# Optimization experiments

Measured on AMD Instinct MI355X. Metric: run time of the kernel, lower is better.

Reference implementation:

```python
import jax, jax.numpy as jnp
import numpy as np

B = 65536
NUM_INPUTS = 128
H0, H1 = 512, 512
K = 200
MIN_W = 0.001
MIN_H = 0.001
MIN_D = 0.001
EDGE_CONST = float(np.log(np.exp(1.0 - 0.001) - 1.0))  # in-place edge derivative value
LN_EPS = 1e-5


def setup_inputs() -> dict:
    key = jax.random.key(0)
    ks = jax.random.split(key, 10)
    f32 = jnp.float32
    inputs = jax.random.normal(ks[0], (B, NUM_INPUTS), dtype=f32)
    W1 = jax.random.normal(ks[1], (H0, NUM_INPUTS), dtype=f32) / np.sqrt(NUM_INPUTS)
    b1 = jnp.zeros((H0,), f32)
    g1 = jnp.ones((H0,), f32)
    be1 = jnp.zeros((H0,), f32)
    W2 = jax.random.normal(ks[2], (H1, H0), dtype=f32) / np.sqrt(H0)
    b2 = jnp.zeros((H1,), f32)
    g2 = jnp.ones((H1,), f32)
    be2 = jnp.zeros((H1,), f32)
    WV = jax.random.normal(ks[3], (3 * K - 1, H1), dtype=f32) / np.sqrt(H1)
    bV = jnp.zeros((3 * K - 1,), f32)
    Wa = jax.random.normal(ks[4], (1, H1), dtype=f32) / np.sqrt(H1)
    ba = jnp.zeros((1,), f32)
    Wb = jax.random.normal(ks[5], (1, H1), dtype=f32) / np.sqrt(H1)
    bb = jnp.zeros((1,), f32)
    return {"inputs": inputs, "W1": W1, "b1": b1, "g1": g1, "be1": be1,
            "W2": W2, "b2": b2, "g2": g2, "be2": be2,
            "WV": WV, "bV": bV, "Wa": Wa, "ba": ba, "Wb": Wb, "bb": bb}


def _layernorm(x, g, b):
    m = jnp.mean(x, axis=-1, keepdims=True)
    v = jnp.mean(jnp.square(x - m), axis=-1, keepdims=True)
    return (x - m) * jax.lax.rsqrt(v + LN_EPS) * g + b


def _spline_forward(inputs, W1, b1, g1, be1, W2, b2, g2, be2, WV, bV, Wa, ba, Wb, bb):
    x = jax.nn.relu(_layernorm(inputs @ W1.T + b1, g1, be1))
    x = jax.nn.relu(_layernorm(x @ W2.T + b2, g2, be2))
    sp = x @ WV.T + bV                      # [B, 3K-1]
    scale_a = jnp.exp(x @ Wa.T + ba)        # [B, 1]
    scale_b = x @ Wb.T + bb                 # [B, 1]

    Wp = jax.nn.softmax(sp[:, :K], axis=1)
    Hp = jax.nn.softmax(sp[:, K:2 * K], axis=1)
    Dp = sp[:, 2 * K:]                      # [B, K-1]
    Wp = MIN_W + (1.0 - MIN_W * K) * Wp
    Hp = MIN_H + (1.0 - MIN_H * K) * Hp
    Dp = MIN_D + jax.nn.softplus(Dp)
    bsz = inputs.shape[0]
    edge = jnp.full((bsz, 1), EDGE_CONST, dtype=inputs.dtype)
    D = jnp.concatenate([edge, Dp, edge], axis=-1)          # [B, K+1]

    zero = jnp.zeros((bsz, 1), dtype=inputs.dtype)
    cw = jnp.concatenate([zero, jnp.cumsum(Wp, axis=-1)], axis=-1)
    cw = cw.at[:, -1].set(1.0)                              # [B, K+1]
    widths = cw[:, 1:] - cw[:, :-1]                         # [B, K]
    ch = jnp.concatenate([zero, jnp.cumsum(Hp, axis=-1)], axis=-1)
    ch = scale_a * ch + scale_b                             # [B, K+1]
    heights = ch[:, 1:] - ch[:, :-1]                        # [B, K]

    tau = ((jnp.arange(K, dtype=inputs.dtype) + 0.5) / K)   # [K]
    tau = jnp.broadcast_to(tau, (bsz, K))

    # sum(tau >= bins) - 1 == searchsorted(bins, tau, side='right') - 1
    bin_idx = jax.vmap(lambda b, t: jnp.searchsorted(b, t, side='right'))(cw, tau) - 1

    ta = lambda a: jnp.take_along_axis(a, bin_idx, axis=-1)
    in_cw = ta(cw)
    in_w = ta(widths)
    in_ch = ta(ch)
    in_h = ta(heights)
    in_delta = ta(heights / widths)
    d0 = ta(D)
    d1 = ta(D[:, 1:])

    theta = (tau - in_cw) / in_w
    t1mt = theta * (1.0 - theta)
    numer = in_h * (in_delta * jnp.square(theta) + d0 * t1mt)
    denom = in_delta + (d0 + d1 - 2.0 * in_delta) * t1mt
    return in_ch + numer / denom            # [B, K]


def reference(inputs, W1, b1, g1, be1, W2, b2, g2, be2, WV, bV, Wa, ba, Wb, bb):
    return _spline_forward(inputs, W1, b1, g1, be1, W2, b2, g2, be2, WV, bV, Wa, ba, Wb, bb)
```

## Files before the change

### kernel.cpp

```cpp
#include <hip/hip_runtime.h>
#include <stdint.h>

typedef __bf16 bf16;
typedef __bf16 bf16x8 __attribute__((ext_vector_type(8)));
typedef __bf16 bf16x4 __attribute__((ext_vector_type(4)));
typedef float  f32x4  __attribute__((ext_vector_type(4)));
typedef uint32_t u32;

#define BATCH    65536
#define NCAT     640
#define SPSTRIDE 604

__device__ __forceinline__ void async16(const void* g, void* l) {
    __builtin_amdgcn_global_load_lds(
        (const u32 __attribute__((address_space(1)))*)g,
        (u32 __attribute__((address_space(3)))*)l,
        16, 0, 0);
}

__global__ __launch_bounds__(256) void prep_kernel(
    const float* W1, const float* W2, const float* WV,
    const float* bV, const float* Wa, const float* ba,
    const float* Wb, const float* bb, const float* inputs,
    bf16* w1b, bf16* w2b, bf16* wcat, float* bcat, bf16* xin)
{
    int idx = blockIdx.x * 256 + threadIdx.x;
    const int n1 = 512 * 128, n2 = 512 * 512, n3 = NCAT * 512;
    const int n5 = BATCH * 128 / 8;
    if (idx < n5) {
        const float4* src = (const float4*)(inputs + idx * 8);
        float4 v0 = src[0], v1 = src[1];
        bf16x8 h;
        h[0]=(bf16)v0.x; h[1]=(bf16)v0.y; h[2]=(bf16)v0.z; h[3]=(bf16)v0.w;
        h[4]=(bf16)v1.x; h[5]=(bf16)v1.y; h[6]=(bf16)v1.z; h[7]=(bf16)v1.w;
        *(bf16x8*)&xin[idx * 8] = h;
        return;
    }
    idx -= n5;
    if (idx < n1) { w1b[idx] = (bf16)W1[idx]; return; }
    idx -= n1;
    if (idx < n2) { w2b[idx] = (bf16)W2[idx]; return; }
    idx -= n2;
    if (idx < n3) {
        int n = idx >> 9, k = idx & 511;
        float v = 0.f;
        if (n < 599)       v = WV[n * 512 + k];
        else if (n == 599) v = Wa[k];
        else if (n == 600) v = Wb[k];
        wcat[idx] = (bf16)v;
        return;
    }
    idx -= n3;
    if (idx < NCAT) {
        float v = 0.f;
        if (idx < 599)       v = bV[idx];
        else if (idx == 599) v = ba[0];
        else if (idx == 600) v = bb[0];
        bcat[idx] = v;
    }
}

template <int KDIM>
__global__ __launch_bounds__(512, 4) void gemm_ln(
    const bf16* __restrict__ A, const bf16* __restrict__ W,
    const float* __restrict__ bias, const float* __restrict__ gamma,
    const float* __restrict__ beta, bf16* out)
{
    __shared__ __align__(16) char smem[8192 + 65536];
    char* Abase = smem;
    char* Bbase = smem + 8192;

    const int t = threadIdx.x;
    const int lane = t & 63, wid = t >> 6;
    const int wm = wid >> 2, wn = wid & 3;
    const int l16 = lane & 15, g16 = lane >> 4;
    const long row0 = (long)blockIdx.x * 64;
    constexpr int NT = KDIM / 32;

    f32x4 acc[2][8];
#pragma unroll
    for (int a = 0; a < 2; ++a)
#pragma unroll
        for (int b = 0; b < 8; ++b) acc[a][b] = (f32x4){0.f, 0.f, 0.f, 0.f};

    auto stageA = [&](int kt, int bi) {
        if (wid < 4) {
            int row = wid * 16 + (lane >> 2);
            const bf16* src = A + (row0 + row) * (long)KDIM + kt * 32 + (lane & 3) * 8;
            async16(src, Abase + bi * 4096 + wid * 1024);
        }
    };
    auto stageB = [&](int kt, int bi) {
#pragma unroll
        for (int c = 0; c < 4; ++c) {
            int call = wid * 4 + c;
            int row = call * 16 + (lane >> 2);
            const bf16* src = W + (long)row * KDIM + kt * 32 + (lane & 3) * 8;
            async16(src, Bbase + bi * 32768 + call * 1024);
        }
    };

    stageA(0, 0); stageB(0, 0);
    __syncthreads();

    for (int kt = 0; kt < NT; ++kt) {
        const int bi = kt & 1;
        if (kt + 1 < NT) { stageA(kt + 1, bi ^ 1); stageB(kt + 1, bi ^ 1); }
        const bf16* Ab = (const bf16*)(Abase + bi * 4096);
        const bf16* Bb = (const bf16*)(Bbase + bi * 32768);
        bf16x8 af[2];
#pragma unroll
        for (int fm = 0; fm < 2; ++fm)
            af[fm] = *(const bf16x8*)(Ab + (wm * 32 + fm * 16 + l16) * 32 + g16 * 8);
#pragma unroll
        for (int fn = 0; fn < 8; ++fn) {
            bf16x8 bv = *(const bf16x8*)(Bb + (wn * 128 + fn * 16 + l16) * 32 + g16 * 8);
            acc[0][fn] = __builtin_amdgcn_mfma_f32_16x16x32_bf16(af[0], bv, acc[0][fn], 0, 0, 0);
            acc[1][fn] = __builtin_amdgcn_mfma_f32_16x16x32_bf16(af[1], bv, acc[1][fn], 0, 0, 0);
        }
        __syncthreads();
    }

    float* Psum = (float*)Abase;
    float* Psq  = (float*)(Abase + 1024);
#pragma unroll
    for (int fm = 0; fm < 2; ++fm)
#pragma unroll
        for (int fn = 0; fn < 8; ++fn) {
            float bv = bias[wn * 128 + fn * 16 + l16];
#pragma unroll
            for (int i = 0; i < 4; ++i) acc[fm][fn][i] += bv;
        }
#pragma unroll
    for (int fm = 0; fm < 2; ++fm)
#pragma unroll
        for (int i = 0; i < 4; ++i) {
            float s = 0.f, q = 0.f;
#pragma unroll
            for (int fn = 0; fn < 8; ++fn) { float v = acc[fm][fn][i]; s += v; q += v * v; }
#pragma unroll
            for (int m = 1; m < 16; m <<= 1) { s += __shfl_xor(s, m); q += __shfl_xor(q, m); }
            if (l16 == 0) {
                int lr = wm * 32 + fm * 16 + g16 * 4 + i;
                Psum[lr * 4 + wn] = s; Psq[lr * 4 + wn] = q;
            }
        }
    __syncthreads();
#pragma unroll
    for (int fm = 0; fm < 2; ++fm)
#pragma unroll
        for (int i = 0; i < 4; ++i) {
            int lr = wm * 32 + fm * 16 + g16 * 4 + i;
            float s = Psum[lr * 4 + 0] + Psum[lr * 4 + 1] + Psum[lr * 4 + 2] + Psum[lr * 4 + 3];
            float q = Psq[lr * 4 + 0] + Psq[lr * 4 + 1] + Psq[lr * 4 + 2] + Psq[lr * 4 + 3];
            float mean = s * (1.f / 512.f);
            float var  = q * (1.f / 512.f) - mean * mean;
            float rstd = rsqrtf(var + 1e-5f);
            long grow = row0 + lr;
#pragma unroll
            for (int fn = 0; fn < 8; ++fn) {
                int col = wn * 128 + fn * 16 + l16;
                float o = (acc[fm][fn][i] - mean) * rstd * gamma[col] + beta[col];
                out[grow * 512 + col] = (bf16)fmaxf(o, 0.f);
            }
        }
}

__global__ __launch_bounds__(512, 4) void gemm_cat(
    const bf16* __restrict__ A, const bf16* __restrict__ W,
    const float* __restrict__ bcat, bf16* __restrict__ sp, float* __restrict__ ab)
{
    __shared__ __align__(16) char smem[16384 + 40960];
    char* Abase = smem;
    char* Bbase = smem + 16384;

    const int t = threadIdx.x;
    const int lane = t & 63, wid = t >> 6;
    const int wm = wid >> 2, wn = wid & 3;
    const int l16 = lane & 15, g16 = lane >> 4;
    const int nh  = blockIdx.x & 1;
    const long row0 = (long)(blockIdx.x >> 1) * 128;

    f32x4 acc[4][5];
#pragma unroll
    for (int a = 0; a < 4; ++a)
#pragma unroll
        for (int b = 0; b < 5; ++b) acc[a][b] = (f32x4){0.f, 0.f, 0.f, 0.f};

    auto stageA = [&](int kt, int bi) {
        int row = wid * 16 + (lane >> 2);
        const bf16* src = A + (row0 + row) * 512 + kt * 32 + (lane & 3) * 8;
        async16(src, Abase + bi * 8192 + wid * 1024);
    };
    auto stageB = [&](int kt, int bi) {
#pragma unroll
        for (int c = 0; c < 3; ++c) {
            int call = c * 8 + wid;
            if (call < 20) {
                int row = nh * 320 + call * 16 + (lane >> 2);
                const bf16* src = W + (long)row * 512 + kt * 32 + (lane & 3) * 8;
                async16(src, Bbase + bi * 20480 + call * 1024);
            }
        }
    };

    stageA(0, 0); stageB(0, 0);
    __syncthreads();

    for (int kt = 0; kt < 16; ++kt) {
        const int bi = kt & 1;
        if (kt < 15) { stageA(kt + 1, bi ^ 1); stageB(kt + 1, bi ^ 1); }
        const bf16* Ab = (const bf16*)(Abase + bi * 8192);
        const bf16* Bb = (const bf16*)(Bbase + bi * 20480);
        bf16x8 af[4];
#pragma unroll
        for (int fm = 0; fm < 4; ++fm)
            af[fm] = *(const bf16x8*)(Ab + (wm * 64 + fm * 16 + l16) * 32 + g16 * 8);
#pragma unroll
        for (int fn = 0; fn < 5; ++fn) {
            bf16x8 bv = *(const bf16x8*)(Bb + (wn * 80 + fn * 16 + l16) * 32 + g16 * 8);
#pragma unroll
            for (int fm = 0; fm < 4; ++fm)
                acc[fm][fn] = __builtin_amdgcn_mfma_f32_16x16x32_bf16(af[fm], bv, acc[fm][fn], 0, 0, 0);
        }
        __syncthreads();
    }

#pragma unroll
    for (int fn = 0; fn < 5; ++fn) {
        int col = nh * 320 + wn * 80 + fn * 16 + l16;
        float bv = (col <= 600) ? bcat[col] : 0.f;
#pragma unroll
        for (int fm = 0; fm < 4; ++fm)
#pragma unroll
            for (int i = 0; i < 4; ++i) {
                long grow = row0 + wm * 64 + fm * 16 + g16 * 4 + i;
                float v = acc[fm][fn][i] + bv;
                if (col < 599)       sp[grow * SPSTRIDE + col] = (bf16)v;
                else if (col == 599) ab[grow * 2 + 0] = v;
                else if (col == 600) ab[grow * 2 + 1] = v;
            }
    }
}

__global__ __launch_bounds__(256) void spline_kernel(
    const bf16* __restrict__ sp, const float* __restrict__ ab, float* __restrict__ out)
{
    __shared__ float S[4][816];
    const int t = threadIdx.x;
    const int lane = t & 63, wid = t >> 6;
    const long row = (long)blockIdx.x * 4 + wid;
    const bf16* spr = sp + row * SPSTRIDE;
    const bool act = lane < 50;
    const float EC = 0.53974247f;
    float* cw = &S[wid][0];
    float* ch = &S[wid][204];
    float* dd = &S[wid][408];
    int*   bx = (int*)&S[wid][612];

    const float sa = __expf(ab[row * 2 + 0]);
    const float sb = ab[row * 2 + 1];

    auto rng = [](float x) -> int {
        int v = (int)ceilf(fmaf(200.f, x, -0.5f));
        return v < 0 ? 0 : (v > 200 ? 200 : v);
    };

    float p0, p1, p2, p3;
    {
        float x0, x1, x2v, x3;
        if (act) {
            bf16x4 v = *(const bf16x4*)&spr[4 * lane];
            x0 = (float)v[0]; x1 = (float)v[1]; x2v = (float)v[2]; x3 = (float)v[3];
        } else { x0 = x1 = x2v = x3 = -1e30f; }
        float m = fmaxf(fmaxf(x0, x1), fmaxf(x2v, x3));
#pragma unroll
        for (int d = 1; d < 64; d <<= 1) m = fmaxf(m, __shfl_xor(m, d));
        float e0 = act ? __expf(x0 - m) : 0.f;
        float e1 = act ? __expf(x1 - m) : 0.f;
        float e2 = act ? __expf(x2v - m) : 0.f;
        float e3 = act ? __expf(x3 - m) : 0.f;
        float s = e0 + e1 + e2 + e3;
#pragma unroll
        for (int d = 1; d < 64; d <<= 1) s += __shfl_xor(s, d);
        float inv = 0.8f / s;
        p0 = act ? fmaf(e0, inv, 0.001f) : 0.f;
        p1 = act ? fmaf(e1, inv, 0.001f) : 0.f;
        p2 = act ? fmaf(e2, inv, 0.001f) : 0.f;
        p3 = act ? fmaf(e3, inv, 0.001f) : 0.f;
    }
    float c0 = p0, c1 = c0 + p1, c2 = c1 + p2, c3 = c2 + p3;
    float run = c3, ts = run;
#pragma unroll
    for (int d = 1; d < 64; d <<= 1) { float u = __shfl_up(ts, d); if (lane >= d) ts += u; }
    float excl  = ts - run;
    float nexcl = __shfl_down(excl, 1);
    float cwl0 = excl, cwl1 = excl + c0, cwl2 = excl + c1, cwl3 = excl + c2;

    float hp0, hp1, hp2, hp3;
    {
        float x0, x1, x2v, x3;
        if (act) {
            bf16x4 v = *(const bf16x4*)&spr[200 + 4 * lane];
            x0 = (float)v[0]; x1 = (float)v[1]; x2v = (float)v[2]; x3 = (float)v[3];
        } else { x0 = x1 = x2v = x3 = -1e30f; }
        float m = fmaxf(fmaxf(x0, x1), fmaxf(x2v, x3));
#pragma unroll
        for (int d = 1; d < 64; d <<= 1) m = fmaxf(m, __shfl_xor(m, d));
        float e0 = act ? __expf(x0 - m) : 0.f;
        float e1 = act ? __expf(x1 - m) : 0.f;
        float e2 = act ? __expf(x2v - m) : 0.f;
        float e3 = act ? __expf(x3 - m) : 0.f;
        float s = e0 + e1 + e2 + e3;
#pragma unroll
        for (int d = 1; d < 64; d <<= 1) s += __shfl_xor(s, d);
        float inv = 0.8f / s;
        hp0 = act ? fmaf(e0, inv, 0.001f) : 0.f;
        hp1 = act ? fmaf(e1, inv, 0.001f) : 0.f;
        hp2 = act ? fmaf(e2, inv, 0.001f) : 0.f;
        hp3 = act ? fmaf(e3, inv, 0.001f) : 0.f;
    }
    float hc0 = hp0, hc1 = hc0 + hp1, hc2 = hc1 + hp2, hc3 = hc2 + hp3;
    float hrun = hc3, hts = hrun;
#pragma unroll
    for (int d = 1; d < 64; d <<= 1) { float u = __shfl_up(hts, d); if (lane >= d) hts += u; }
    float hexcl = hts - hrun;
    float ch0 = fmaf(sa, hexcl, sb);
    float ch1 = fmaf(sa, hexcl + hc0, sb);
    float ch2 = fmaf(sa, hexcl + hc1, sb);
    float ch3 = fmaf(sa, hexcl + hc2, sb);

    float dv0, dv1, dv2, dv3;
    {
        float x0 = 0.f, x1 = 0.f, x2v = 0.f, x3 = 0.f;
        if (act) {
            bf16x4 v = *(const bf16x4*)&spr[400 + 4 * lane];
            x0 = (float)v[0]; x1 = (float)v[1]; x2v = (float)v[2]; x3 = (float)v[3];
        }
        auto spls = [](float x) {
            return fmaxf(x, 0.f) + __logf(1.f + __expf(-fabsf(x))) + 0.001f;
        };
        dv0 = spls(x0); dv1 = spls(x1); dv2 = spls(x2v); dv3 = spls(x3);
    }
    if (lane == 49) dv3 = EC;
    float dprev = __shfl_up(dv3, 1);
    if (lane == 0) dprev = EC;

    if (act) {
        *(f32x4*)&cw[4 * lane] = (f32x4){cwl0, cwl1, cwl2, cwl3};
        *(f32x4*)&ch[4 * lane] = (f32x4){ch0, ch1, ch2, ch3};
        *(f32x4*)&dd[4 * lane] = (f32x4){dprev, dv0, dv1, dv2};
    }
    if (lane == 49) {
        cw[200] = 1.0f;
        ch[200] = fmaf(sa, hts, sb);
        dd[200] = EC;
    }

    if (act) {
        int b0 = rng(cwl0), b1 = rng(cwl1), b2 = rng(cwl2), b3 = rng(cwl3);
        int b4 = (lane == 49) ? 200 : rng(nexcl);
        for (int j = b0; j < b1; ++j) bx[j] = 4 * lane;
        for (int j = b1; j < b2; ++j) bx[j] = 4 * lane + 1;
        for (int j = b2; j < b3; ++j) bx[j] = 4 * lane + 2;
        for (int j = b3; j < b4; ++j) bx[j] = 4 * lane + 3;
    }
    asm volatile("s_waitcnt lgkmcnt(0)" ::: "memory");

    if (act) {
        float* orow = out + (size_t)row * 200;
#pragma unroll
        for (int k = 0; k < 4; ++k) {
            int j = lane + 50 * k;
            int b = bx[j];
            float wl = cw[b], wr = cw[b + 1];
            float hl = ch[b], hr = ch[b + 1];
            float d0 = dd[b], d1 = dd[b + 1];
            float tau = ((float)j + 0.5f) * (1.f / 200.f);
            float w = wr - wl, h = hr - hl;
            float invw = 1.f / w;
            float delta = h * invw;
            float th = (tau - wl) * invw;
            float t1 = th * (1.f - th);
            float numer = h * fmaf(delta * th, th, d0 * t1);
            float denom = fmaf(d0 + d1 - 2.f * delta, t1, delta);
            orow[j] = hl + numer / denom;
        }
    }
}

extern "C" void kernel_launch(void* const* d_in, const int* in_sizes, int n_in,
                              void* d_out, int out_size, void* d_ws, size_t ws_size,
                              hipStream_t stream)
{
    const float* inputs = (const float*)d_in[0];
    const float* W1  = (const float*)d_in[1];
    const float* b1  = (const float*)d_in[2];
    const float* g1  = (const float*)d_in[3];
    const float* be1 = (const float*)d_in[4];
    const float* W2  = (const float*)d_in[5];
    const float* b2  = (const float*)d_in[6];
    const float* g2  = (const float*)d_in[7];
    const float* be2 = (const float*)d_in[8];
    const float* WV  = (const float*)d_in[9];
    const float* bV  = (const float*)d_in[10];
    const float* Wa  = (const float*)d_in[11];
    const float* ba  = (const float*)d_in[12];
    const float* Wb  = (const float*)d_in[13];
    const float* bb  = (const float*)d_in[14];
    float* out = (float*)d_out;

    char* ws = (char*)d_ws;
    bf16*  w1b  = (bf16*) (ws + 0);
    bf16*  w2b  = (bf16*) (ws + 131072);
    bf16*  wcat = (bf16*) (ws + 655360);
    float* bcat = (float*)(ws + 1310720);
    float* ab   = (float*)(ws + 1313280);
    bf16*  x    = (bf16*) (ws + 2097152);
    bf16*  spb  = (bf16*) (ws + 69206016);
    bf16*  xin  = (bf16*) (ws + 69206016);

    const int preptot = BATCH * 128 / 8 + 512 * 128 + 512 * 512 + NCAT * 512 + NCAT;
    prep_kernel<<<(preptot + 255) / 256, 256, 0, stream>>>(
        W1, W2, WV, bV, Wa, ba, Wb, bb, inputs, w1b, w2b, wcat, bcat, xin);

    gemm_ln<128><<<BATCH / 64, 512, 0, stream>>>(xin, w1b, b1, g1, be1, x);
    gemm_ln<512><<<BATCH / 64, 512, 0, stream>>>(x,   w2b, b2, g2, be2, x);
    gemm_cat<<<(BATCH / 128) * 2, 512, 0, stream>>>(x, wcat, bcat, spb, ab);
    spline_kernel<<<BATCH / 4, 256, 0, stream>>>(spb, ab, out);
}
```

Baseline: 258.5 us.

## Stage GEMM epilogue outputs through LDS for coalesced stores; halve gemm_cat row tile

The LayerNorm GEMM epilogue now writes its bf16 results into shared memory, then stores full rows back with 16-byte vector writes instead of scattered 2-byte stores. gemm_cat does the same through an LDS staging tile and writes 8-byte chunks into the padded sp buffer. gemm_cat's row tile drops from 128 to 64, which doubles the grid and lowers per-block LDS and register use. The cost is an extra block-wide sync and an LDS round trip per block, and each gemm_cat block now does less compute per B-tile load.

Result: faster. 250.1 us (-3.2%).

```diff
diff --git a/kernel.cpp b/kernel.cpp
--- a/kernel.cpp
+++ b/kernel.cpp
@@ -123,6 +123,7 @@
 
     float* Psum = (float*)Abase;
     float* Psq  = (float*)(Abase + 1024);
+    bf16*  stg  = (bf16*)Bbase;
 #pragma unroll
     for (int fm = 0; fm < 2; ++fm)
 #pragma unroll
@@ -156,41 +157,49 @@
             float mean = s * (1.f / 512.f);
             float var  = q * (1.f / 512.f) - mean * mean;
             float rstd = rsqrtf(var + 1e-5f);
-            long grow = row0 + lr;
 #pragma unroll
             for (int fn = 0; fn < 8; ++fn) {
                 int col = wn * 128 + fn * 16 + l16;
                 float o = (acc[fm][fn][i] - mean) * rstd * gamma[col] + beta[col];
-                out[grow * 512 + col] = (bf16)fmaxf(o, 0.f);
+                stg[lr * 512 + col] = (bf16)fmaxf(o, 0.f);
             }
         }
+    __syncthreads();
+#pragma unroll
+    for (int i = 0; i < 8; ++i) {
+        int idx = i * 512 + t;
+        *(bf16x8*)&out[(row0 + (idx >> 6)) * 512 + (idx & 63) * 8] =
+            *(const bf16x8*)&stg[idx * 8];
+    }
 }
 
 __global__ __launch_bounds__(512, 4) void gemm_cat(
     const bf16* __restrict__ A, const bf16* __restrict__ W,
     const float* __restrict__ bcat, bf16* __restrict__ sp, float* __restrict__ ab)
 {
-    __shared__ __align__(16) char smem[16384 + 40960];
+    __shared__ __align__(16) char smem[8192 + 40960];
     char* Abase = smem;
-    char* Bbase = smem + 16384;
+    char* Bbase = smem + 8192;
 
     const int t = threadIdx.x;
     const int lane = t & 63, wid = t >> 6;
     const int wm = wid >> 2, wn = wid & 3;
     const int l16 = lane & 15, g16 = lane >> 4;
     const int nh  = blockIdx.x & 1;
-    const long row0 = (long)(blockIdx.x >> 1) * 128;
-
-    f32x4 acc[4][5];
-#pragma unroll
-    for (int a = 0; a < 4; ++a)
+    const long row0 = (long)(blockIdx.x >> 1) * 64;
+
+    f32x4 acc[2][5];
+#pragma unroll
+    for (int a = 0; a < 2; ++a)
 #pragma unroll
         for (int b = 0; b < 5; ++b) acc[a][b] = (f32x4){0.f, 0.f, 0.f, 0.f};
 
     auto stageA = [&](int kt, int bi) {
-        int row = wid * 16 + (lane >> 2);
-        const bf16* src = A + (row0 + row) * 512 + kt * 32 + (lane & 3) * 8;
-        async16(src, Abase + bi * 8192 + wid * 1024);
+        if (wid < 4) {
+            int row = wid * 16 + (lane >> 2);
+            const bf16* src = A + (row0 + row) * 512 + kt * 32 + (lane & 3) * 8;
+            async16(src, Abase + bi * 4096 + wid * 1024);
+        }
     };
     auto stageB = [&](int kt, int bi) {
 #pragma unroll
@@ -210,36 +219,51 @@
     for (int kt = 0; kt < 16; ++kt) {
         const int bi = kt & 1;
         if (kt < 15) { stageA(kt + 1, bi ^ 1); stageB(kt + 1, bi ^ 1); }
-        const bf16* Ab = (const bf16*)(Abase + bi * 8192);
+        const bf16* Ab = (const bf16*)(Abase + bi * 4096);
         const bf16* Bb = (const bf16*)(Bbase + bi * 20480);
-        bf16x8 af[4];
-#pragma unroll
-        for (int fm = 0; fm < 4; ++fm)
-            af[fm] = *(const bf16x8*)(Ab + (wm * 64 + fm * 16 + l16) * 32 + g16 * 8);
+        bf16x8 af[2];
+#pragma unroll
+        for (int fm = 0; fm < 2; ++fm)
+            af[fm] = *(const bf16x8*)(Ab + (wm * 32 + fm * 16 + l16) * 32 + g16 * 8);
 #pragma unroll
         for (int fn = 0; fn < 5; ++fn) {
             bf16x8 bv = *(const bf16x8*)(Bb + (wn * 80 + fn * 16 + l16) * 32 + g16 * 8);
-#pragma unroll
-            for (int fm = 0; fm < 4; ++fm)
-                acc[fm][fn] = __builtin_amdgcn_mfma_f32_16x16x32_bf16(af[fm], bv, acc[fm][fn], 0, 0, 0);
+            acc[0][fn] = __builtin_amdgcn_mfma_f32_16x16x32_bf16(af[0], bv, acc[0][fn], 0, 0, 0);
+            acc[1][fn] = __builtin_amdgcn_mfma_f32_16x16x32_bf16(af[1], bv, acc[1][fn], 0, 0, 0);
         }
         __syncthreads();
     }
 
+    bf16* stg = (bf16*)smem;
 #pragma unroll
     for (int fn = 0; fn < 5; ++fn) {
-        int col = nh * 320 + wn * 80 + fn * 16 + l16;
-        float bv = (col <= 600) ? bcat[col] : 0.f;
-#pragma unroll
-        for (int fm = 0; fm < 4; ++fm)
+        int lcol = wn * 80 + fn * 16 + l16;
+        int col  = nh * 320 + lcol;
+        float bv = bcat[col];
+#pragma unroll
+        for (int fm = 0; fm < 2; ++fm)
 #pragma unroll
             for (int i = 0; i < 4; ++i) {
-                long grow = row0 + wm * 64 + fm * 16 + g16 * 4 + i;
+                int r = wm * 32 + fm * 16 + g16 * 4 + i;
                 float v = acc[fm][fn][i] + bv;
-                if (col < 599)       sp[grow * SPSTRIDE + col] = (bf16)v;
-                else if (col == 599) ab[grow * 2 + 0] = v;
-                else if (col == 600) ab[grow * 2 + 1] = v;
+                stg[r * 320 + lcol] = (bf16)v;
+                if (col == 599)      ab[(row0 + r) * 2 + 0] = v;
+                else if (col == 600) ab[(row0 + r) * 2 + 1] = v;
             }
+    }
+    __syncthreads();
+    if (nh == 0) {
+        for (int c = t; c < 64 * 80; c += 512) {
+            int r = c / 80, k = c % 80;
+            *(uint64_t*)&sp[(row0 + r) * SPSTRIDE + k * 4] =
+                *(const uint64_t*)&stg[r * 320 + k * 4];
+        }
+    } else {
+        for (int c = t; c < 64 * 70; c += 512) {
+            int r = c / 70, k = c % 70;
+            *(uint64_t*)&sp[(row0 + r) * SPSTRIDE + 320 + k * 4] =
+                *(const uint64_t*)&stg[r * 320 + k * 4];
+        }
     }
 }
 
@@ -426,6 +450,6 @@
 
     gemm_ln<128><<<BATCH / 64, 512, 0, stream>>>(xin, w1b, b1, g1, be1, x);
     gemm_ln<512><<<BATCH / 64, 512, 0, stream>>>(x,   w2b, b2, g2, be2, x);
-    gemm_cat<<<(BATCH / 128) * 2, 512, 0, stream>>>(x, wcat, bcat, spb, ab);
+    gemm_cat<<<(BATCH / 64) * 2, 512, 0, stream>>>(x, wcat, bcat, spb, ab);
     spline_kernel<<<BATCH / 4, 256, 0, stream>>>(spb, ab, out);
 }
```
